# Optimization experiments

Hardware: AMD Instinct MI355X
Metric: run time of the kernel (lower is better)

## Reference

```python
import jax, jax.numpy as jnp
from jax import lax
import numpy as np

DN = ('NCHW', 'OIHW', 'NCHW')

def _conv(x, w, b, s, p):
    out = lax.conv_general_dilated(x, w, (s, s), ((p, p), (p, p)), dimension_numbers=DN)
    return out + b[None, :, None, None]

def _convt(x, w, b):
    # torch ConvTranspose2d(k=3, stride=2, pad=1, out_pad=1) == lhs-dilated conv
    # with flipped kernel, pad (k-1-p, k-1-p+op) = (1, 2). Doubles H, W.
    wk = jnp.flip(w, (2, 3)).transpose(1, 0, 2, 3)  # [Cin,Cout,k,k] -> [Cout,Cin,k,k]
    out = lax.conv_general_dilated(x, wk, (1, 1), ((1, 2), (1, 2)), lhs_dilation=(2, 2), dimension_numbers=DN)
    return out + b[None, :, None, None]

def _bn(x, g, b):
    # training-mode batch stats over (N, H, W), eps=1e-5
    m = jnp.mean(x, (0, 2, 3), keepdims=True)
    v = jnp.var(x, (0, 2, 3), keepdims=True)
    return (x - m) * lax.rsqrt(v + 1e-5) * g[None, :, None, None] + b[None, :, None, None]

def _hsw(x):
    return x * jnp.clip(x + 3.0, 0.0, 6.0) * (1.0 / 6.0)

SCORE_THRESHOLD = 0.6
DOWN_SCALE = 4.0

def _forward(feature, ch_w1, ch_b1, ch_w2, ch_b2, ch_w3, ch_b3, ch_g1, ch_be1, ch_g2, ch_be2,
             cl_w1, cl_b1, cl_w2, cl_b2, cl_g, cl_be, cl_dw, cl_db,
             rg_tw, rg_tb, rg_g, rg_be, rg_w, rg_b, hm_tw, hm_tb):
    # ---- CommonHead (note: original reuses bn1 after both stride-2 convs) ----
    h = _bn(_conv(feature, ch_w1, ch_b1, 2, 1), ch_g1, ch_be1)   # [B,192,64,64]
    h = _bn(_conv(h, ch_w2, ch_b2, 2, 1), ch_g1, ch_be1)         # [B,192,32,32]
    h = _hsw(_bn(_conv(h, ch_w3, ch_b3, 1, 0), ch_g2, ch_be2))   # [B,32,32,32]
    # ---- PageClassifyNet ----
    c = _hsw(_bn(_conv(h, cl_w1, cl_b1, 1, 1), cl_g, cl_be))     # [B,32,32,32]
    c = _conv(c, cl_w2, cl_b2, 1, 1)                             # [B,1,32,32]
    cls = c.reshape(c.shape[0], -1) @ cl_dw.T + cl_db            # [B,2]
    r = _hsw(_bn(_convt(feature, rg_tw, rg_tb), rg_g, rg_be))    # [B,32,256,256]
    reg = _conv(r, rg_w, rg_b, 1, 1)                             # [B,2,256,256]
    # ---- AuxiliaryHeatmapNet ----
    hm = _convt(feature, hm_tw, hm_tb)                           # [B,8,256,256]
    # ---- keypoint decode (threshold + argmax + gather), vectorized over batch ----
    B, _, H, W = hm.shape
    flat = hm.transpose(0, 2, 3, 1).reshape(B, H * W, 8)          # HWC layout as in source
    pages = jnp.stack([flat[..., :4], flat[..., 4:]], axis=1)     # [B,2(pages),HW,4(corners)]
    idx = jnp.argmax(pages, axis=2)                               # [B,2,4] flat spatial index
    y_idx = (idx // W).astype(reg.dtype)
    x_idx = (idx % W).astype(reg.dtype)
    fi = idx.reshape(B, -1)                                       # [B,8]
    reg_flat = reg.reshape(B, 2, H * W)
    off_x = jnp.take_along_axis(reg_flat[:, 0, :], fi, axis=1).reshape(B, 2, 4)
    off_y = jnp.take_along_axis(reg_flat[:, 1, :], fi, axis=1).reshape(B, 2, 4)
    xs = jnp.clip((off_x + x_idx) * DOWN_SCALE / (W * DOWN_SCALE), 0.0, 1.0)
    ys = jnp.clip((off_y + y_idx) * DOWN_SCALE / (H * DOWN_SCALE), 0.0, 1.0)
    valid = cls > SCORE_THRESHOLD                                 # [B,2]
    label = jnp.broadcast_to(jnp.arange(2, dtype=xs.dtype)[None, :], (B, 2))
    row = jnp.concatenate([label[..., None], xs, ys], axis=-1)    # [B,2,9]
    return jnp.where(valid[..., None], row, jnp.asarray(-1.0, xs.dtype))


def setup_inputs() -> dict:
    key = jax.random.key(0)
    ks = jax.random.split(key, 32)
    rn = lambda k, shp, s=0.05: jax.random.normal(k, shp, dtype=jnp.float32) * s
    d = {}
    d['feature'] = jax.random.normal(ks[0], (8, 512, 128, 128), dtype=jnp.float32)
    d['ch_w1'] = rn(ks[1], (192, 512, 3, 3)); d['ch_b1'] = rn(ks[2], (192,))
    d['ch_w2'] = rn(ks[3], (192, 192, 3, 3)); d['ch_b2'] = rn(ks[4], (192,))
    d['ch_w3'] = rn(ks[5], (32, 192, 1, 1)); d['ch_b3'] = rn(ks[6], (32,))
    d['ch_g1'] = jnp.ones((192,), jnp.float32); d['ch_be1'] = jnp.zeros((192,), jnp.float32)
    d['ch_g2'] = jnp.ones((32,), jnp.float32); d['ch_be2'] = jnp.zeros((32,), jnp.float32)
    d['cl_w1'] = rn(ks[7], (32, 32, 3, 3)); d['cl_b1'] = rn(ks[8], (32,))
    d['cl_w2'] = rn(ks[9], (1, 32, 3, 3)); d['cl_b2'] = rn(ks[10], (1,))
    d['cl_g'] = jnp.ones((32,), jnp.float32); d['cl_be'] = jnp.zeros((32,), jnp.float32)
    d['cl_dw'] = rn(ks[11], (2, 1024), 0.1); d['cl_db'] = rn(ks[12], (2,))
    d['rg_tw'] = rn(ks[13], (512, 32, 3, 3)); d['rg_tb'] = rn(ks[14], (32,))
    d['rg_g'] = jnp.ones((32,), jnp.float32); d['rg_be'] = jnp.zeros((32,), jnp.float32)
    d['rg_w'] = rn(ks[15], (2, 32, 3, 3)); d['rg_b'] = rn(ks[16], (2,))
    d['hm_tw'] = rn(ks[17], (512, 8, 3, 3)); d['hm_tb'] = rn(ks[18], (8,))
    return d


def reference(feature, ch_w1, ch_b1, ch_w2, ch_b2, ch_w3, ch_b3, ch_g1, ch_be1, ch_g2, ch_be2,
              cl_w1, cl_b1, cl_w2, cl_b2, cl_g, cl_be, cl_dw, cl_db,
              rg_tw, rg_tb, rg_g, rg_be, rg_w, rg_b, hm_tw, hm_tb):
    return _forward(feature, ch_w1, ch_b1, ch_w2, ch_b2, ch_w3, ch_b3, ch_g1, ch_be1, ch_g2, ch_be2,
                    cl_w1, cl_b1, cl_w2, cl_b2, cl_g, cl_be, cl_dw, cl_db,
                    rg_tw, rg_tb, rg_g, rg_be, rg_w, rg_b, hm_tw, hm_tb)
```

## Files before the change

kernel.cpp:

```cpp
#include <hip/hip_runtime.h>

typedef unsigned short u16;
typedef u16 u16x4 __attribute__((ext_vector_type(4)));
typedef u16 u16x8 __attribute__((ext_vector_type(8)));
typedef __bf16 bf16x8 __attribute__((ext_vector_type(8)));
typedef float f32x4 __attribute__((ext_vector_type(4)));

__device__ __forceinline__ float bf2f(u16 v) {
  unsigned u = ((unsigned)v) << 16;
  return __builtin_bit_cast(float, u);
}
__device__ __forceinline__ u16 f2bf(float f) {
  unsigned u = __builtin_bit_cast(unsigned, f);
  u += 0x7FFFu + ((u >> 16) & 1u);
  return (u16)(u >> 16);
}
__device__ __forceinline__ float hsw(float v) {
  return v * fminf(fmaxf(v + 3.f, 0.f), 6.f) * (1.f / 6.f);
}
__device__ __forceinline__ f32x4 mfma16(u16x8 a, u16x8 b, f32x4 c) {
  return __builtin_amdgcn_mfma_f32_16x16x32_bf16(
      __builtin_bit_cast(bf16x8, a), __builtin_bit_cast(bf16x8, b), c, 0, 0, 0);
}

#define LR 40

__global__ __launch_bounds__(256) void k_tobf(const float* __restrict__ f,
                                              u16* __restrict__ fbh) {
  __shared__ float tl[64 * 65];
  const int t = threadIdx.x;
  const int bid = blockIdx.x;
  const int ict = bid & 7, xt = (bid >> 3) & 1, y = (bid >> 4) & 127, n = bid >> 11;
  const int x0 = xt * 64, ic0 = ict * 64;
#pragma unroll
  for (int i = 0; i < 4; ++i) {
    const int e = t + i * 256;
    const int icl = e >> 4, xq = e & 15;
    const f32x4 v =
        *(const f32x4*)&f[((n * 512 + ic0 + icl) * 128 + y) * 128 + x0 + xq * 4];
#pragma unroll
    for (int j = 0; j < 4; ++j) tl[icl * 65 + xq * 4 + j] = v[j];
  }
  __syncthreads();
#pragma unroll
  for (int i = 0; i < 4; ++i) {
    const int e = t + i * 256;
    const int xl = e >> 4;
    const int icg = (e & 15) * 4;
    u16x4 v;
#pragma unroll
    for (int j = 0; j < 4; ++j) v[j] = f2bf(tl[(icg + j) * 65 + xl]);
    *(u16x4*)&fbh[(((size_t)((n * 128 + y) * 128 + x0 + xl)) << 9) + ic0 + icg] = v;
  }
}

__global__ __launch_bounds__(256) void k_pack_all(const float* __restrict__ w1,
                                                  const float* __restrict__ w2,
                                                  const float* __restrict__ rgw,
                                                  const float* __restrict__ hmw,
                                                  u16* __restrict__ bp1,
                                                  u16* __restrict__ bp2,
                                                  u16* __restrict__ bp5) {
  const int b = blockIdx.x;
  if (b < 3456) {
    const int e = b * 256 + threadIdx.x;
    const int ici = e & 31;
    const int rest = e >> 5;
    const int oc = rest % 192;
    const int kc = rest / 192;
    const int icc = kc & 15, tap = kc >> 4;
    const int ic = icc * 32 + ici;
    bp1[e] = f2bf(w1[(oc * 512 + ic) * 9 + tap]);
  } else if (b < 4752) {
    const int e = (b - 3456) * 256 + threadIdx.x;
    const int ici = e & 31;
    const int rest = e >> 5;
    const int oc = rest % 192;
    const int kc = rest / 192;
    const int icc = kc % 6, tap = kc / 6;
    const int ic = icc * 32 + ici;
    bp2[e] = f2bf(w2[(oc * 192 + ic) * 9 + tap]);
  } else {
    const int e = (b - 4752) * 256 + threadIdx.x;
    const int ici = e & 31;
    const int rest = e >> 5;
    const int oc = rest % 48;
    const int sic = rest / 48;
    const int icc = sic & 15, slot = sic >> 4;
    const int ic = icc * 32 + ici;
    const int kytab[9] = {1, 1, 1, 2, 0, 2, 2, 0, 0};
    const int kxtab[9] = {1, 2, 0, 1, 1, 2, 0, 2, 0};
    const int ky = kytab[slot], kx = kxtab[slot];
    float v = 0.f;
    if (oc < 32)
      v = rgw[((ic * 32 + oc) * 3 + ky) * 3 + kx];
    else if (oc < 40)
      v = hmw[((ic * 8 + (oc - 32)) * 3 + ky) * 3 + kx];
    bp5[e] = f2bf(v);
  }
}

__global__ __launch_bounds__(256) void k_conv1(const u16* __restrict__ fbh,
                                               const u16* __restrict__ bph,
                                               const float* __restrict__ bias,
                                               u16* __restrict__ y1) {
  __shared__ u16 Al[64 * LR];
  __shared__ u16 Bl[192 * LR];
  __shared__ float bl[192];
  const int t = threadIdx.x;
  const int n = blockIdx.x >> 6, oy = blockIdx.x & 63;
  if (t < 192) bl[t] = bias[t];
  const int lane = t & 63, wv = t >> 6;
  const int row = lane & 15, g = lane >> 4;
  const int oxs = t >> 2, icq = t & 3;
  const f32x4 z4 = {0.f, 0.f, 0.f, 0.f};
  f32x4 acc[4][3];
#pragma unroll
  for (int i = 0; i < 4; ++i)
#pragma unroll
    for (int j = 0; j < 3; ++j) acc[i][j] = z4;

#define C1_LOAD(KC, AV, BV)                                                    \
  {                                                                            \
    const int tap_ = (KC) >> 4, icc_ = (KC)&15;                                \
    const int ky_ = tap_ / 3, kx_ = tap_ - ky_ * 3;                            \
    const int iy_ = 2 * oy - 1 + ky_;                                          \
    const int ix_ = 2 * oxs - 1 + kx_;                                         \
    u16x8 v_ = {0, 0, 0, 0, 0, 0, 0, 0};                                       \
    if ((unsigned)iy_ < 128u && (unsigned)ix_ < 128u)                          \
      v_ = *(const u16x8*)&fbh[((size_t)((n * 128 + iy_) * 128 + ix_) << 9) +  \
                               icc_ * 32 + icq * 8];                           \
    AV = v_;                                                                   \
    const size_t bbase_ = (size_t)(tap_ * 16 + icc_) * (192 * 32);             \
    _Pragma("unroll") for (int i_ = 0; i_ < 3; ++i_) {                         \
      const int e_ = t + i_ * 256;                                             \
      BV[i_] = *(const u16x8*)&bph[bbase_ + (e_ >> 2) * 32 + (e_ & 3) * 8];    \
    }                                                                          \
  }

  u16x8 avA, bvA[3], avB, bvB[3];
  C1_LOAD(0, avA, bvA);

  for (int kc = 0; kc < 144; ++kc) {
    __syncthreads();
    *(u16x8*)&Al[oxs * LR + icq * 8] = avA;
#pragma unroll
    for (int i = 0; i < 3; ++i) {
      const int e = t + i * 256;
      *(u16x8*)&Bl[(e >> 2) * LR + (e & 3) * 8] = bvA[i];
    }
    __syncthreads();
    if (kc < 143) C1_LOAD(kc + 1, avB, bvB);
    u16x8 af[4], bf[3];
#pragma unroll
    for (int mf = 0; mf < 4; ++mf)
      af[mf] = *(const u16x8*)&Al[(mf * 16 + row) * LR + g * 8];
#pragma unroll
    for (int nf = 0; nf < 3; ++nf)
      bf[nf] = *(const u16x8*)&Bl[(wv * 48 + nf * 16 + row) * LR + g * 8];
#pragma unroll
    for (int mf = 0; mf < 4; ++mf)
#pragma unroll
      for (int nf = 0; nf < 3; ++nf) acc[mf][nf] = mfma16(af[mf], bf[nf], acc[mf][nf]);
    avA = avB;
#pragma unroll
    for (int i = 0; i < 3; ++i) bvA[i] = bvB[i];
  }
#undef C1_LOAD
#pragma unroll
  for (int mf = 0; mf < 4; ++mf)
#pragma unroll
    for (int nf = 0; nf < 3; ++nf)
#pragma unroll
      for (int r = 0; r < 4; ++r) {
        const int m = mf * 16 + g * 4 + r;
        const int oc = wv * 48 + nf * 16 + row;
        y1[((n * 64 + oy) * 64 + m) * 192 + oc] = f2bf(acc[mf][nf][r] + bl[oc]);
      }
}

__global__ __launch_bounds__(256) void k_conv2(const u16* __restrict__ y1,
                                               const u16* __restrict__ bph,
                                               const float* __restrict__ bias,
                                               const float* __restrict__ sc,
                                               const float* __restrict__ sh,
                                               float* __restrict__ y2) {
  __shared__ u16 Al[64 * LR];
  __shared__ u16 Bl[192 * LR];
  __shared__ float bl[192], scl[192], shl[192];
  const int t = threadIdx.x;
  const int n = blockIdx.x >> 4, oyp = blockIdx.x & 15;
  if (t < 192) {
    bl[t] = bias[t];
    scl[t] = sc[t];
    shl[t] = sh[t];
  }
  __syncthreads();
  const int lane = t & 63, wv = t >> 6;
  const int row = lane & 15, g = lane >> 4;
  const int ms = t >> 2, icq = t & 3;
  const int ryr = ms >> 5, oxs = ms & 31;
  const f32x4 z4 = {0.f, 0.f, 0.f, 0.f};
  f32x4 acc[4][3];
#pragma unroll
  for (int i = 0; i < 4; ++i)
#pragma unroll
    for (int j = 0; j < 3; ++j) acc[i][j] = z4;

#define C2_LOAD(KC, RAW, OK, BV)                                               \
  {                                                                            \
    const int tap_ = (KC) / 6, icc_ = (KC)-tap_ * 6;                           \
    const int ky_ = tap_ / 3, kx_ = tap_ - ky_ * 3;                            \
    const int iy_ = 2 * (oyp * 2 + ryr) - 1 + ky_;                             \
    const int ix_ = 2 * oxs - 1 + kx_;                                         \
    OK = ((unsigned)iy_ < 64u) && ((unsigned)ix_ < 64u);                       \
    u16x8 v_ = {0, 0, 0, 0, 0, 0, 0, 0};                                       \
    if (OK)                                                                    \
      v_ = *(const u16x8*)&y1[((n * 64 + iy_) * 64 + ix_) * 192 + icc_ * 32 +  \
                              icq * 8];                                        \
    RAW = v_;                                                                  \
    const size_t bbase_ = (size_t)(tap_ * 6 + icc_) * (192 * 32);              \
    _Pragma("unroll") for (int i_ = 0; i_ < 3; ++i_) {                         \
      const int e_ = t + i_ * 256;                                             \
      BV[i_] = *(const u16x8*)&bph[bbase_ + (e_ >> 2) * 32 + (e_ & 3) * 8];    \
    }                                                                          \
  }

  u16x8 rawA, bvA[3], rawB, bvB[3];
  bool okA, okB;
  C2_LOAD(0, rawA, okA, bvA);

  for (int kc = 0; kc < 54; ++kc) {
    const int tap = kc / 6, icc = kc - tap * 6;
    const int icb = icc * 32 + icq * 8;
    u16x8 av = {0, 0, 0, 0, 0, 0, 0, 0};
    if (okA) {
#pragma unroll
      for (int j = 0; j < 8; ++j)
        av[j] = f2bf(bf2f(rawA[j]) * scl[icb + j] + shl[icb + j]);
    }
    __syncthreads();
    *(u16x8*)&Al[ms * LR + icq * 8] = av;
#pragma unroll
    for (int i = 0; i < 3; ++i) {
      const int e = t + i * 256;
      *(u16x8*)&Bl[(e >> 2) * LR + (e & 3) * 8] = bvA[i];
    }
    __syncthreads();
    if (kc < 53) C2_LOAD(kc + 1, rawB, okB, bvB);
    u16x8 af[4], bf[3];
#pragma unroll
    for (int mf = 0; mf < 4; ++mf)
      af[mf] = *(const u16x8*)&Al[(mf * 16 + row) * LR + g * 8];
#pragma unroll
    for (int nf = 0; nf < 3; ++nf)
      bf[nf] = *(const u16x8*)&Bl[(wv * 48 + nf * 16 + row) * LR + g * 8];
#pragma unroll
    for (int mf = 0; mf < 4; ++mf)
#pragma unroll
      for (int nf = 0; nf < 3; ++nf) acc[mf][nf] = mfma16(af[mf], bf[nf], acc[mf][nf]);
    rawA = rawB;
    okA = okB;
#pragma unroll
    for (int i = 0; i < 3; ++i) bvA[i] = bvB[i];
  }
#undef C2_LOAD
#pragma unroll
  for (int mf = 0; mf < 4; ++mf)
#pragma unroll
    for (int nf = 0; nf < 3; ++nf)
#pragma unroll
      for (int r = 0; r < 4; ++r) {
        const int m = mf * 16 + g * 4 + r;
        const int oy = oyp * 2 + (m >> 5), ox = m & 31;
        const int oc = wv * 48 + nf * 16 + row;
        y2[((n * 32 + oy) * 32 + ox) * 192 + oc] = acc[mf][nf][r] + bl[oc];
      }
}

#define AST 40
#define ARS (130 * 40)
#define BST 40
__global__ __launch_bounds__(256) void k_convt(const u16* __restrict__ fbh,
                                               const u16* __restrict__ bph,
                                               const float* __restrict__ rgb,
                                               const float* __restrict__ hmb,
                                               u16* __restrict__ rr,
                                               float* __restrict__ hm) {
  __shared__ u16 AH[2 * ARS];
  __shared__ u16 BH[9 * 48 * BST];
  const int t = threadIdx.x;
  const int bid = (blockIdx.x & 7) * 128 + (blockIdx.x >> 3);
  const int n = bid >> 7, iyb = bid & 127;
  const int lane = t & 63, wv = t >> 6;
  const int row = lane & 15, g = lane >> 4;

  if (t < 8) {
    const int r = t >> 2, j = t & 3;
    const u16x8 z = {0, 0, 0, 0, 0, 0, 0, 0};
    *(u16x8*)&AH[r * ARS + 128 * AST + j * 8] = z;
  }

  float bias3[3];
#pragma unroll
  for (int nf = 0; nf < 3; ++nf) {
    const int oc = nf * 16 + row;
    bias3[nf] = (oc < 32) ? rgb[oc] : ((oc < 40) ? hmb[oc - 32] : 0.f);
  }

  const int SCt[9] = {0, 1, 1, 2, 2, 3, 3, 3, 3};
  const int SDt[9] = {0, 0, 0, 0, 1, 0, 0, 1, 1};
  const int SXt[9] = {0, 0, 1, 0, 0, 0, 1, 0, 1};

  int rr_[4], px_[4], iq_[4];
#pragma unroll
  for (int i = 0; i < 4; ++i) {
    const int u = t + i * 256;
    rr_[i] = u >> 9;
    px_[i] = (u >> 2) & 127;
    iq_[i] = u & 3;
  }

  const f32x4 z4 = {0.f, 0.f, 0.f, 0.f};
  f32x4 acc[4][2][3];
#pragma unroll
  for (int c = 0; c < 4; ++c)
#pragma unroll
    for (int m = 0; m < 2; ++m)
#pragma unroll
      for (int j = 0; j < 3; ++j) acc[c][m][j] = z4;

#define LOAD_A(ICC, DST)                                                       \
  _Pragma("unroll") for (int i = 0; i < 4; ++i) {                              \
    const int iy = iyb + rr_[i];                                               \
    u16x8 v = {0, 0, 0, 0, 0, 0, 0, 0};                                        \
    if (iy < 128)                                                              \
      v = *(const u16x8*)&fbh[((size_t)((n * 128 + iy) * 128 + px_[i]) << 9) + \
                              (ICC)*32 + iq_[i] * 8];                          \
    DST[i] = v;                                                                \
  }

#define LOAD_B(ICC, DST)                                                       \
  _Pragma("unroll") for (int i = 0; i < 7; ++i) {                              \
    const int e = t + i * 256;                                                 \
    u16x8 v = {0, 0, 0, 0, 0, 0, 0, 0};                                        \
    if (e < 1728) {                                                            \
      const int slot = e / 192, rem = e % 192;                                 \
      const int oc = rem >> 2, icq = rem & 3;                                  \
      v = *(const u16x8*)&bph[((size_t)((slot * 16 + (ICC)) * 48 + oc) << 5) + \
                              icq * 8];                                        \
    }                                                                          \
    DST[i] = v;                                                                \
  }

  u16x8 ahA[4], bhA[7], ahB[4], bhB[7];
  LOAD_A(0, ahA);
  LOAD_B(0, bhA);

  for (int icc = 0; icc < 16; ++icc) {
    __syncthreads();
#pragma unroll
    for (int i = 0; i < 4; ++i)
      *(u16x8*)&AH[rr_[i] * ARS + px_[i] * AST + iq_[i] * 8] = ahA[i];
#pragma unroll
    for (int i = 0; i < 7; ++i) {
      const int e = t + i * 256;
      if (e < 1728) {
        const int slot = e / 192, rem = e % 192;
        const int oc = rem >> 2, icq = rem & 3;
        *(u16x8*)&BH[(slot * 48 + oc) * BST + icq * 8] = bhA[i];
      }
    }
    __syncthreads();

    if (icc < 15) {
      LOAD_A(icc + 1, ahB);
      LOAD_B(icc + 1, bhB);
    }

#pragma unroll
    for (int slot = 0; slot < 9; ++slot) {
      const int cls = SCt[slot], diy = SDt[slot], dix = SXt[slot];
      const u16x8 bf0 = *(const u16x8*)&BH[(slot * 48 + row) * BST + g * 8];
      const u16x8 bf1 = *(const u16x8*)&BH[(slot * 48 + 16 + row) * BST + g * 8];
      const u16x8 bf2 = *(const u16x8*)&BH[(slot * 48 + 32 + row) * BST + g * 8];
#pragma unroll
      for (int mfl = 0; mfl < 2; ++mfl) {
        const int mf = wv * 2 + mfl;
        const u16x8 af =
            *(const u16x8*)&AH[diy * ARS + (mf * 16 + row + dix) * AST + g * 8];
        acc[cls][mfl][0] = mfma16(af, bf0, acc[cls][mfl][0]);
        acc[cls][mfl][1] = mfma16(af, bf1, acc[cls][mfl][1]);
        acc[cls][mfl][2] = mfma16(af, bf2, acc[cls][mfl][2]);
      }
    }

#pragma unroll
    for (int i = 0; i < 4; ++i) ahA[i] = ahB[i];
#pragma unroll
    for (int i = 0; i < 7; ++i) bhA[i] = bhB[i];
  }
#undef LOAD_A
#undef LOAD_B

#pragma unroll
  for (int cls = 0; cls < 4; ++cls) {
    const int oy = 2 * iyb + (cls >> 1);
    const int xp = cls & 1;
#pragma unroll
    for (int mfl = 0; mfl < 2; ++mfl)
#pragma unroll
      for (int nf = 0; nf < 3; ++nf)
#pragma unroll
        for (int r = 0; r < 4; ++r) {
          const int m = (wv * 2 + mfl) * 16 + g * 4 + r;
          const int ox = 2 * m + xp;
          const int oc = nf * 16 + row;
          const float v = acc[cls][mfl][nf][r] + bias3[nf];
          if (oc < 32)
            rr[((size_t)((n * 256 + oy) * 256 + ox)) * 32 + oc] = f2bf(v);
          else if (oc < 40)
            hm[(size_t)(n * 8 + (oc - 32)) * 65536 + oy * 256 + ox] = v;
        }
  }
}

template <int CG, bool BF16>
__global__ __launch_bounds__(256) void k_statsf(
    const void* __restrict__ in_, int M, int PB, float* __restrict__ gsum,
    float* __restrict__ gsq, int* __restrict__ counter,
    const float* __restrict__ g, const float* __restrict__ be, float invM,
    float* __restrict__ sc, float* __restrict__ sh) {
  const int C = CG * 32;
  __shared__ float red[8][CG * 32];
  __shared__ int lastBlk;
  const int t = threadIdx.x;
  const int pg = t >> 5, ln = t & 31;
  float s[CG], q[CG];
#pragma unroll
  for (int c = 0; c < CG; ++c) { s[c] = 0.f; q[c] = 0.f; }
  const int p0 = blockIdx.x * PB;
  const int pend = min(p0 + PB, M);
  for (int p = p0 + pg; p < pend; p += 8) {
#pragma unroll
    for (int c = 0; c < CG; ++c) {
      float v;
      if (BF16)
        v = bf2f(((const u16*)in_)[(size_t)p * C + c * 32 + ln]);
      else
        v = ((const float*)in_)[(size_t)p * C + c * 32 + ln];
      s[c] += v;
      q[c] += v * v;
    }
  }
#pragma unroll
  for (int c = 0; c < CG; ++c) red[pg][c * 32 + ln] = s[c];
  __syncthreads();
  if (t < C) {
    float tot = 0.f;
#pragma unroll
    for (int k = 0; k < 8; ++k) tot += red[k][t];
    atomicAdd(&gsum[t], tot);
  }
  __syncthreads();
#pragma unroll
  for (int c = 0; c < CG; ++c) red[pg][c * 32 + ln] = q[c];
  __syncthreads();
  if (t < C) {
    float tot = 0.f;
#pragma unroll
    for (int k = 0; k < 8; ++k) tot += red[k][t];
    atomicAdd(&gsq[t], tot);
  }
  __syncthreads();
  if (t == 0) {
    __threadfence();
    lastBlk = (atomicAdd(counter, 1) == (int)gridDim.x - 1) ? 1 : 0;
  }
  __syncthreads();
  if (lastBlk) {
    __threadfence();
    if (t < C) {
      const float m = gsum[t] * invM;
      const float var = gsq[t] * invM - m * m;
      const float inv = rsqrtf(var + 1e-5f);
      const float sg = g[t] * inv;
      sc[t] = sg;
      sh[t] = be[t] - m * sg;
    }
  }
}

__global__ __launch_bounds__(256) void k_conv3(const float* __restrict__ y2,
                                               const float* __restrict__ w3,
                                               const float* __restrict__ b3,
                                               const float* __restrict__ sc,
                                               const float* __restrict__ sh,
                                               float* __restrict__ y3) {
  __shared__ float wl[32 * 192];
  __shared__ float scl[192], shl[192];
  const int t = threadIdx.x;
  for (int e = t; e < 6144; e += 256) wl[e] = w3[e];
  if (t < 192) {
    scl[t] = sc[t];
    shl[t] = sh[t];
  }
  __syncthreads();
  const int px = blockIdx.x * 256 + t;
  float acc[32];
#pragma unroll
  for (int oc = 0; oc < 32; ++oc) acc[oc] = 0.f;
  const float* base = &y2[(size_t)px * 192];
  for (int icb = 0; icb < 192; icb += 8) {
    const f32x4 r0 = *(const f32x4*)&base[icb];
    const f32x4 r1 = *(const f32x4*)&base[icb + 4];
    float v[8];
#pragma unroll
    for (int j = 0; j < 8; ++j) {
      const float r = (j < 4) ? r0[j & 3] : r1[j & 3];
      v[j] = r * scl[icb + j] + shl[icb + j];
    }
#pragma unroll
    for (int oc = 0; oc < 32; ++oc) {
      const f32x4 w0 = *(const f32x4*)&wl[oc * 192 + icb];
      const f32x4 w1 = *(const f32x4*)&wl[oc * 192 + icb + 4];
      acc[oc] += v[0] * w0[0] + v[1] * w0[1] + v[2] * w0[2] + v[3] * w0[3] +
                 v[4] * w1[0] + v[5] * w1[1] + v[6] * w1[2] + v[7] * w1[3];
    }
  }
#pragma unroll
  for (int oc = 0; oc < 32; ++oc) y3[(size_t)px * 32 + oc] = acc[oc] + b3[oc];
}

__global__ __launch_bounds__(256) void k_clsconv1(const float* __restrict__ y3,
                                                  const float* __restrict__ w1,
                                                  const float* __restrict__ b1,
                                                  const float* __restrict__ sc,
                                                  const float* __restrict__ sh,
                                                  float* __restrict__ c1) {
  __shared__ float wl[9216];
  __shared__ float scl[32], shl[32];
  const int t = threadIdx.x;
  for (int e = t; e < 9216; e += 256) {
    const int oc = e & 31;
    const int tmp = e >> 5;
    const int tap = tmp % 9, ic = tmp / 9;
    wl[e] = w1[(oc * 32 + ic) * 9 + tap];
  }
  if (t < 32) {
    scl[t] = sc[t];
    shl[t] = sh[t];
  }
  __syncthreads();
  const int px = blockIdx.x * 64 + (t & 63);
  const int ocg = t >> 6;
  const int n = px >> 10, y0 = (px >> 5) & 31, x0 = px & 31;
  float acc[8];
#pragma unroll
  for (int j = 0; j < 8; ++j) acc[j] = 0.f;
  for (int tap = 0; tap < 9; ++tap) {
    const int dy = tap / 3 - 1, dx = tap % 3 - 1;
    const int yy = y0 + dy, xx = x0 + dx;
    if ((unsigned)yy < 32u && (unsigned)xx < 32u) {
      const float* ib = &y3[((n << 10) + yy * 32 + xx) * 32];
      for (int ic = 0; ic < 32; ++ic) {
        const float v = hsw(ib[ic] * scl[ic] + shl[ic]);
        const float* wp = &wl[(ic * 9 + tap) * 32 + ocg * 8];
#pragma unroll
        for (int j = 0; j < 8; ++j) acc[j] += v * wp[j];
      }
    }
  }
#pragma unroll
  for (int j = 0; j < 8; ++j) c1[px * 32 + ocg * 8 + j] = acc[j] + b1[ocg * 8 + j];
}

__global__ __launch_bounds__(256) void k_cls(const float* __restrict__ c1,
                                             const float* __restrict__ w2,
                                             const float* __restrict__ b2,
                                             const float* __restrict__ dw,
                                             const float* __restrict__ db,
                                             const float* __restrict__ sc,
                                             const float* __restrict__ sh,
                                             float* __restrict__ cls) {
  __shared__ float wl[288];
  __shared__ float scl[32], shl[32];
  __shared__ float red0[256], red1[256];
  const int t = threadIdx.x;
  const int n = blockIdx.x;
  for (int e = t; e < 288; e += 256) wl[e] = w2[e];
  if (t < 32) {
    scl[t] = sc[t];
    shl[t] = sh[t];
  }
  __syncthreads();
  float s0 = 0.f, s1 = 0.f;
  for (int i = 0; i < 4; ++i) {
    const int px = i * 256 + t;
    const int y0 = px >> 5, x0 = px & 31;
    float c2 = b2[0];
    for (int tap = 0; tap < 9; ++tap) {
      const int dy = tap / 3 - 1, dx = tap % 3 - 1;
      const int yy = y0 + dy, xx = x0 + dx;
      if ((unsigned)yy < 32u && (unsigned)xx < 32u) {
        const float* ib = &c1[((n << 10) + yy * 32 + xx) * 32];
        for (int ic = 0; ic < 32; ++ic)
          c2 += hsw(ib[ic] * scl[ic] + shl[ic]) * wl[ic * 9 + tap];
      }
    }
    s0 += c2 * dw[px];
    s1 += c2 * dw[1024 + px];
  }
  red0[t] = s0;
  red1[t] = s1;
  __syncthreads();
  for (int s = 128; s; s >>= 1) {
    if (t < s) {
      red0[t] += red0[t + s];
      red1[t] += red1[t + s];
    }
    __syncthreads();
  }
  if (t == 0) {
    cls[n * 2 + 0] = red0[0] + db[0];
    cls[n * 2 + 1] = red1[0] + db[1];
  }
}

__global__ __launch_bounds__(256) void k_regconv(const u16* __restrict__ rr,
                                                 const float* __restrict__ w,
                                                 const float* __restrict__ b,
                                                 const float* __restrict__ sc,
                                                 const float* __restrict__ sh,
                                                 float* __restrict__ reg) {
  __shared__ u16 rl[3 * 258 * 33];
  __shared__ float wl[576];
  __shared__ float scl[32], shl[32];
  const int t = threadIdx.x;
  const int n = blockIdx.x >> 8, oy = blockIdx.x & 255;
  for (int e = t; e < 576; e += 256) wl[e] = w[e];
  if (t < 32) {
    scl[t] = sc[t];
    shl[t] = sh[t];
  }
  if (t < 192) {
    const int ry = t / 64, side = (t >> 5) & 1, ic = t & 31;
    rl[(ry * 258 + side * 257) * 33 + ic] = 0;
  }
  __syncthreads();
  for (int e = t; e < 3072; e += 256) {
    const int icq8 = e & 3;
    const int pxx = (e >> 2) & 255;
    const int ry = e >> 10;
    const int rowi = oy - 1 + ry;
    u16x8 raw = {0, 0, 0, 0, 0, 0, 0, 0};
    bool ok = (unsigned)rowi < 256u;
    if (ok)
      raw = *(const u16x8*)&rr[((size_t)((n * 256 + rowi) * 256 + pxx)) * 32 + icq8 * 8];
#pragma unroll
    for (int j = 0; j < 8; ++j) {
      const int ic = icq8 * 8 + j;
      float v = 0.f;
      if (ok) v = hsw(bf2f(raw[j]) * scl[ic] + shl[ic]);
      rl[(ry * 258 + pxx + 1) * 33 + ic] = f2bf(v);
    }
  }
  __syncthreads();
  const int px = t;
  float a0 = b[0], a1 = b[1];
#pragma unroll
  for (int ry = 0; ry < 3; ++ry)
#pragma unroll
    for (int kx = 0; kx < 3; ++kx) {
      const u16* ib = &rl[(ry * 258 + px + kx) * 33];
      for (int ic = 0; ic < 32; ++ic) {
        const float v = bf2f(ib[ic]);
        a0 += v * wl[ic * 9 + ry * 3 + kx];
        a1 += v * wl[288 + ic * 9 + ry * 3 + kx];
      }
    }
  reg[(n * 2 + 0) * 65536 + oy * 256 + px] = a0;
  reg[(n * 2 + 1) * 65536 + oy * 256 + px] = a1;
}

__global__ __launch_bounds__(256) void k_argmaxfin(const float* __restrict__ hm,
                                                   int* __restrict__ idx,
                                                   int* __restrict__ counter,
                                                   const float* __restrict__ cls,
                                                   const float* __restrict__ reg,
                                                   float* __restrict__ out) {
  __shared__ float bv[256];
  __shared__ int bi[256];
  __shared__ int lastBlk;
  const int t = threadIdx.x;
  const float* base = &hm[(size_t)blockIdx.x * 65536];
  float best = -3.402823466e38f;
  int bidx = 2147483647;
  for (int i = t; i < 65536; i += 256) {
    const float v = base[i];
    if (v > best) {
      best = v;
      bidx = i;
    }
  }
  bv[t] = best;
  bi[t] = bidx;
  __syncthreads();
  for (int s = 128; s; s >>= 1) {
    if (t < s) {
      if (bv[t + s] > bv[t] || (bv[t + s] == bv[t] && bi[t + s] < bi[t])) {
        bv[t] = bv[t + s];
        bi[t] = bi[t + s];
      }
    }
    __syncthreads();
  }
  if (t == 0) {
    idx[blockIdx.x] = bi[0];
    __threadfence();
    lastBlk = (atomicAdd(counter, 1) == (int)gridDim.x - 1) ? 1 : 0;
  }
  __syncthreads();
  if (lastBlk) {
    __threadfence();
    if (t < 16) {
      const int n = t >> 1, p = t & 1;
      const float cv = cls[n * 2 + p];
      float* o = &out[(n * 2 + p) * 9];
      if (!(cv > 0.6f)) {
        for (int i = 0; i < 9; ++i) o[i] = -1.f;
      } else {
        o[0] = (float)p;
        for (int c = 0; c < 4; ++c) {
          const int id = idx[n * 8 + p * 4 + c];
          const int yi = id >> 8, xi = id & 255;
          const float ox_ = reg[(n * 2 + 0) * 65536 + id];
          const float oy_ = reg[(n * 2 + 1) * 65536 + id];
          o[1 + c] = fminf(fmaxf((ox_ + (float)xi) * (1.f / 256.f), 0.f), 1.f);
          o[5 + c] = fminf(fmaxf((oy_ + (float)yi) * (1.f / 256.f), 0.f), 1.f);
        }
      }
    }
  }
}

extern "C" void kernel_launch(void* const* d_in, const int* in_sizes, int n_in,
                              void* d_out, int out_size, void* d_ws, size_t ws_size,
                              hipStream_t stream) {
  const float* feature = (const float*)d_in[0];
  const float* ch_w1 = (const float*)d_in[1];
  const float* ch_b1 = (const float*)d_in[2];
  const float* ch_w2 = (const float*)d_in[3];
  const float* ch_b2 = (const float*)d_in[4];
  const float* ch_w3 = (const float*)d_in[5];
  const float* ch_b3 = (const float*)d_in[6];
  const float* ch_g1 = (const float*)d_in[7];
  const float* ch_be1 = (const float*)d_in[8];
  const float* ch_g2 = (const float*)d_in[9];
  const float* ch_be2 = (const float*)d_in[10];
  const float* cl_w1 = (const float*)d_in[11];
  const float* cl_b1 = (const float*)d_in[12];
  const float* cl_w2 = (const float*)d_in[13];
  const float* cl_b2 = (const float*)d_in[14];
  const float* cl_g = (const float*)d_in[15];
  const float* cl_be = (const float*)d_in[16];
  const float* cl_dw = (const float*)d_in[17];
  const float* cl_db = (const float*)d_in[18];
  const float* rg_tw = (const float*)d_in[19];
  const float* rg_tb = (const float*)d_in[20];
  const float* rg_g = (const float*)d_in[21];
  const float* rg_be = (const float*)d_in[22];
  const float* rg_w = (const float*)d_in[23];
  const float* rg_b = (const float*)d_in[24];
  const float* hm_tw = (const float*)d_in[25];
  const float* hm_tb = (const float*)d_in[26];
  float* out = (float*)d_out;

  char* w = (char*)d_ws;
  const size_t OFF_FB = 0;
  const size_t OFF_BP1 = 134217728;
  const size_t OFF_BP2 = 135987200;
  const size_t OFF_BP5 = 136650752;
  const size_t OFF_Y1 = 137093120;
  const size_t OFF_Y2 = 149676032;
  const size_t OFF_Y3 = 155967488;
  const size_t OFF_C1 = 157016064;
  const size_t OFF_RR = 158064640;
  const size_t OFF_HM = 191619072;
  const size_t OFF_REG = 208396288;
  const size_t OFF_STATS = 212590592;
  const size_t OFF_PARAMS = 212594496;
  const size_t OFF_CLS = 212598336;
  const size_t OFF_IDX = 212598400;
  const size_t WS_NEED = 212598656;
  if (ws_size < WS_NEED) return;

  u16* FB = (u16*)(w + OFF_FB);
  u16* BP1 = (u16*)(w + OFF_BP1);
  u16* BP2 = (u16*)(w + OFF_BP2);
  u16* BP5 = (u16*)(w + OFF_BP5);
  u16* Y1 = (u16*)(w + OFF_Y1);
  float* Y2 = (float*)(w + OFF_Y2);
  float* Y3 = (float*)(w + OFF_Y3);
  float* C1 = (float*)(w + OFF_C1);
  u16* RR = (u16*)(w + OFF_RR);
  float* HM = (float*)(w + OFF_HM);
  float* REG = (float*)(w + OFF_REG);
  float* GSUM = (float*)(w + OFF_STATS);
  float* GSQ = GSUM + 480;
  int* CNT = (int*)(w + OFF_STATS + 3840);
  float* SC = (float*)(w + OFF_PARAMS);
  float* SH = SC + 480;
  float* CLS = (float*)(w + OFF_CLS);
  int* IDX = (int*)(w + OFF_IDX);

  (void)hipMemsetAsync(w + OFF_STATS, 0, 3904, stream);

  k_tobf<<<16384, 256, 0, stream>>>(feature, FB);
  k_pack_all<<<5616, 256, 0, stream>>>(ch_w1, ch_w2, rg_tw, hm_tw, BP1, BP2, BP5);

  k_conv1<<<512, 256, 0, stream>>>(FB, BP1, ch_b1, Y1);
  k_statsf<6, true><<<128, 256, 0, stream>>>(Y1, 32768, 256, GSUM + 0, GSQ + 0,
                                             CNT + 0, ch_g1, ch_be1, 1.f / 32768.f,
                                             SC + 0, SH + 0);
  k_conv2<<<128, 256, 0, stream>>>(Y1, BP2, ch_b2, SC + 0, SH + 0, Y2);
  k_statsf<6, false><<<32, 256, 0, stream>>>(Y2, 8192, 256, GSUM + 192, GSQ + 192,
                                             CNT + 1, ch_g1, ch_be1, 1.f / 8192.f,
                                             SC + 192, SH + 192);
  k_conv3<<<32, 256, 0, stream>>>(Y2, ch_w3, ch_b3, SC + 192, SH + 192, Y3);
  k_statsf<1, false><<<8, 256, 0, stream>>>(Y3, 8192, 1024, GSUM + 384, GSQ + 384,
                                            CNT + 2, ch_g2, ch_be2, 1.f / 8192.f,
                                            SC + 384, SH + 384);
  k_clsconv1<<<128, 256, 0, stream>>>(Y3, cl_w1, cl_b1, SC + 384, SH + 384, C1);
  k_statsf<1, false><<<8, 256, 0, stream>>>(C1, 8192, 1024, GSUM + 416, GSQ + 416,
                                            CNT + 3, cl_g, cl_be, 1.f / 8192.f,
                                            SC + 416, SH + 416);
  k_cls<<<8, 256, 0, stream>>>(C1, cl_w2, cl_b2, cl_dw, cl_db, SC + 416, SH + 416,
                               CLS);
  k_convt<<<1024, 256, 0, stream>>>(FB, BP5, rg_tb, hm_tb, RR, HM);
  k_statsf<1, true><<<256, 256, 0, stream>>>(RR, 524288, 2048, GSUM + 448, GSQ + 448,
                                             CNT + 4, rg_g, rg_be, 1.f / 524288.f,
                                             SC + 448, SH + 448);
  k_regconv<<<2048, 256, 0, stream>>>(RR, rg_w, rg_b, SC + 448, SH + 448, REG);
  k_argmaxfin<<<64, 256, 0, stream>>>(HM, IDX, CNT + 5, CLS, REG, out);
}
```

Measured before the change: 809.5 us.

## Fuse BatchNorm statistics into conv1, conv2 and convT epilogues

Each of the three conv kernels now accumulates per-channel sum and sum-of-squares in its epilogue. Partials are reduced in shared memory, then added atomically to global buffers, and the last block computes the BN scale and shift. This removes three separate stats kernels, their launches, and the re-read of the conv outputs (the convT output is large). In exchange it adds global atomics, fence and counter logic to each conv, and computes the stats from fp32 values instead of the rounded bf16 stored outputs.

Measured after the change: 768.5 us. 5.1% less time.

```diff
diff --git a/kernel.cpp b/kernel.cpp
--- a/kernel.cpp
+++ b/kernel.cpp
@@ -103,13 +103,26 @@
 __global__ __launch_bounds__(256) void k_conv1(const u16* __restrict__ fbh,
                                                const u16* __restrict__ bph,
                                                const float* __restrict__ bias,
-                                               u16* __restrict__ y1) {
+                                               u16* __restrict__ y1,
+                                               float* __restrict__ gsum,
+                                               float* __restrict__ gsq,
+                                               int* __restrict__ counter,
+                                               const float* __restrict__ g1,
+                                               const float* __restrict__ be1,
+                                               float* __restrict__ sc,
+                                               float* __restrict__ sh) {
   __shared__ u16 Al[64 * LR];
   __shared__ u16 Bl[192 * LR];
   __shared__ float bl[192];
+  __shared__ float ssum[192], ssq[192];
+  __shared__ int lastBlk;
   const int t = threadIdx.x;
   const int n = blockIdx.x >> 6, oy = blockIdx.x & 63;
-  if (t < 192) bl[t] = bias[t];
+  if (t < 192) {
+    bl[t] = bias[t];
+    ssum[t] = 0.f;
+    ssq[t] = 0.f;
+  }
   const int lane = t & 63, wv = t >> 6;
   const int row = lane & 15, g = lane >> 4;
   const int oxs = t >> 2, icq = t & 3;
@@ -167,6 +180,8 @@
     for (int i = 0; i < 3; ++i) bvA[i] = bvB[i];
   }
 #undef C1_LOAD
+
+  float s3[3] = {0.f, 0.f, 0.f}, q3[3] = {0.f, 0.f, 0.f};
 #pragma unroll
   for (int mf = 0; mf < 4; ++mf)
 #pragma unroll
@@ -175,25 +190,67 @@
       for (int r = 0; r < 4; ++r) {
         const int m = mf * 16 + g * 4 + r;
         const int oc = wv * 48 + nf * 16 + row;
-        y1[((n * 64 + oy) * 64 + m) * 192 + oc] = f2bf(acc[mf][nf][r] + bl[oc]);
+        const float v = acc[mf][nf][r] + bl[oc];
+        y1[((n * 64 + oy) * 64 + m) * 192 + oc] = f2bf(v);
+        s3[nf] += v;
+        q3[nf] += v * v;
       }
+#pragma unroll
+  for (int nf = 0; nf < 3; ++nf) {
+    const int oc = wv * 48 + nf * 16 + row;
+    atomicAdd(&ssum[oc], s3[nf]);
+    atomicAdd(&ssq[oc], q3[nf]);
+  }
+  __syncthreads();
+  if (t < 192) {
+    atomicAdd(&gsum[t], ssum[t]);
+    atomicAdd(&gsq[t], ssq[t]);
+  }
+  __syncthreads();
+  if (t == 0) {
+    __threadfence();
+    lastBlk = (atomicAdd(counter, 1) == (int)gridDim.x - 1) ? 1 : 0;
+  }
+  __syncthreads();
+  if (lastBlk) {
+    __threadfence();
+    if (t < 192) {
+      const float m = gsum[t] * (1.f / 32768.f);
+      const float var = gsq[t] * (1.f / 32768.f) - m * m;
+      const float inv = rsqrtf(var + 1e-5f);
+      const float sg = g1[t] * inv;
+      sc[t] = sg;
+      sh[t] = be1[t] - m * sg;
+    }
+  }
 }
 
 __global__ __launch_bounds__(256) void k_conv2(const u16* __restrict__ y1,
                                                const u16* __restrict__ bph,
                                                const float* __restrict__ bias,
-                                               const float* __restrict__ sc,
-                                               const float* __restrict__ sh,
-                                               float* __restrict__ y2) {
+                                               const float* __restrict__ sc_in,
+                                               const float* __restrict__ sh_in,
+                                               float* __restrict__ y2,
+                                               float* __restrict__ gsum,
+                                               float* __restrict__ gsq,
+                                               int* __restrict__ counter,
+                                               const float* __restrict__ g1,
+                                               const float* __restrict__ be1,
+                                               float* __restrict__ sc,
+                                               float* __restrict__ sh) {
   __shared__ u16 Al[64 * LR];
   __shared__ u16 Bl[192 * LR];
   __shared__ float bl[192], scl[192], shl[192];
+  __shared__ float ssum[192], ssq[192];
+  __shared__ int lastBlk;
   const int t = threadIdx.x;
   const int n = blockIdx.x >> 4, oyp = blockIdx.x & 15;
   if (t < 192) {
     bl[t] = bias[t];
-    scl[t] = sc[t];
-    shl[t] = sh[t];
+    scl[t] = sc_in[t];
+    shl[t] = sh_in[t];
+    ssum[t] = 0.f;
+    ssq[t] = 0.f;
   }
   __syncthreads();
   const int lane = t & 63, wv = t >> 6;
@@ -265,6 +322,8 @@
     for (int i = 0; i < 3; ++i) bvA[i] = bvB[i];
   }
 #undef C2_LOAD
+
+  float s3[3] = {0.f, 0.f, 0.f}, q3[3] = {0.f, 0.f, 0.f};
 #pragma unroll
   for (int mf = 0; mf < 4; ++mf)
 #pragma unroll
@@ -274,8 +333,39 @@
         const int m = mf * 16 + g * 4 + r;
         const int oy = oyp * 2 + (m >> 5), ox = m & 31;
         const int oc = wv * 48 + nf * 16 + row;
-        y2[((n * 32 + oy) * 32 + ox) * 192 + oc] = acc[mf][nf][r] + bl[oc];
+        const float v = acc[mf][nf][r] + bl[oc];
+        y2[((n * 32 + oy) * 32 + ox) * 192 + oc] = v;
+        s3[nf] += v;
+        q3[nf] += v * v;
       }
+#pragma unroll
+  for (int nf = 0; nf < 3; ++nf) {
+    const int oc = wv * 48 + nf * 16 + row;
+    atomicAdd(&ssum[oc], s3[nf]);
+    atomicAdd(&ssq[oc], q3[nf]);
+  }
+  __syncthreads();
+  if (t < 192) {
+    atomicAdd(&gsum[t], ssum[t]);
+    atomicAdd(&gsq[t], ssq[t]);
+  }
+  __syncthreads();
+  if (t == 0) {
+    __threadfence();
+    lastBlk = (atomicAdd(counter, 1) == (int)gridDim.x - 1) ? 1 : 0;
+  }
+  __syncthreads();
+  if (lastBlk) {
+    __threadfence();
+    if (t < 192) {
+      const float m = gsum[t] * (1.f / 8192.f);
+      const float var = gsq[t] * (1.f / 8192.f) - m * m;
+      const float inv = rsqrtf(var + 1e-5f);
+      const float sg = g1[t] * inv;
+      sc[t] = sg;
+      sh[t] = be1[t] - m * sg;
+    }
+  }
 }
 
 #define AST 40
@@ -286,9 +376,18 @@
                                                const float* __restrict__ rgb,
                                                const float* __restrict__ hmb,
                                                u16* __restrict__ rr,
-                                               float* __restrict__ hm) {
+                                               float* __restrict__ hm,
+                                               float* __restrict__ gsum,
+                                               float* __restrict__ gsq,
+                                               int* __restrict__ counter,
+                                               const float* __restrict__ rg_g,
+                                               const float* __restrict__ rg_be,
+                                               float* __restrict__ sc,
+                                               float* __restrict__ sh) {
   __shared__ u16 AH[2 * ARS];
   __shared__ u16 BH[9 * 48 * BST];
+  __shared__ float ssum[32], ssq[32];
+  __shared__ int lastBlk;
   const int t = threadIdx.x;
   const int bid = (blockIdx.x & 7) * 128 + (blockIdx.x >> 3);
   const int n = bid >> 7, iyb = bid & 127;
@@ -299,6 +398,10 @@
     const int r = t >> 2, j = t & 3;
     const u16x8 z = {0, 0, 0, 0, 0, 0, 0, 0};
     *(u16x8*)&AH[r * ARS + 128 * AST + j * 8] = z;
+  }
+  if (t < 32) {
+    ssum[t] = 0.f;
+    ssq[t] = 0.f;
   }
 
   float bias3[3];
@@ -403,6 +506,7 @@
 #undef LOAD_A
 #undef LOAD_B
 
+  float s2[2] = {0.f, 0.f}, q2[2] = {0.f, 0.f};
 #pragma unroll
   for (int cls = 0; cls < 4; ++cls) {
     const int oy = 2 * iyb + (cls >> 1);
@@ -417,11 +521,40 @@
           const int ox = 2 * m + xp;
           const int oc = nf * 16 + row;
           const float v = acc[cls][mfl][nf][r] + bias3[nf];
-          if (oc < 32)
+          if (oc < 32) {
             rr[((size_t)((n * 256 + oy) * 256 + ox)) * 32 + oc] = f2bf(v);
-          else if (oc < 40)
+            s2[nf] += v;
+            q2[nf] += v * v;
+          } else if (oc < 40)
             hm[(size_t)(n * 8 + (oc - 32)) * 65536 + oy * 256 + ox] = v;
         }
+  }
+#pragma unroll
+  for (int nf = 0; nf < 2; ++nf) {
+    atomicAdd(&ssum[nf * 16 + row], s2[nf]);
+    atomicAdd(&ssq[nf * 16 + row], q2[nf]);
+  }
+  __syncthreads();
+  if (t < 32) {
+    atomicAdd(&gsum[t], ssum[t]);
+    atomicAdd(&gsq[t], ssq[t]);
+  }
+  __syncthreads();
+  if (t == 0) {
+    __threadfence();
+    lastBlk = (atomicAdd(counter, 1) == (int)gridDim.x - 1) ? 1 : 0;
+  }
+  __syncthreads();
+  if (lastBlk) {
+    __threadfence();
+    if (t < 32) {
+      const float m = gsum[t] * (1.f / 524288.f);
+      const float var = gsq[t] * (1.f / 524288.f) - m * m;
+      const float inv = rsqrtf(var + 1e-5f);
+      const float sg = rg_g[t] * inv;
+      sc[t] = sg;
+      sh[t] = rg_be[t] - m * sg;
+    }
   }
 }
 
@@ -819,14 +952,11 @@
   k_tobf<<<16384, 256, 0, stream>>>(feature, FB);
   k_pack_all<<<5616, 256, 0, stream>>>(ch_w1, ch_w2, rg_tw, hm_tw, BP1, BP2, BP5);
 
-  k_conv1<<<512, 256, 0, stream>>>(FB, BP1, ch_b1, Y1);
-  k_statsf<6, true><<<128, 256, 0, stream>>>(Y1, 32768, 256, GSUM + 0, GSQ + 0,
-                                             CNT + 0, ch_g1, ch_be1, 1.f / 32768.f,
-                                             SC + 0, SH + 0);
-  k_conv2<<<128, 256, 0, stream>>>(Y1, BP2, ch_b2, SC + 0, SH + 0, Y2);
-  k_statsf<6, false><<<32, 256, 0, stream>>>(Y2, 8192, 256, GSUM + 192, GSQ + 192,
-                                             CNT + 1, ch_g1, ch_be1, 1.f / 8192.f,
-                                             SC + 192, SH + 192);
+  k_conv1<<<512, 256, 0, stream>>>(FB, BP1, ch_b1, Y1, GSUM + 0, GSQ + 0, CNT + 0,
+                                   ch_g1, ch_be1, SC + 0, SH + 0);
+  k_conv2<<<128, 256, 0, stream>>>(Y1, BP2, ch_b2, SC + 0, SH + 0, Y2, GSUM + 192,
+                                   GSQ + 192, CNT + 1, ch_g1, ch_be1, SC + 192,
+                                   SH + 192);
   k_conv3<<<32, 256, 0, stream>>>(Y2, ch_w3, ch_b3, SC + 192, SH + 192, Y3);
   k_statsf<1, false><<<8, 256, 0, stream>>>(Y3, 8192, 1024, GSUM + 384, GSQ + 384,
                                             CNT + 2, ch_g2, ch_be2, 1.f / 8192.f,
@@ -837,10 +967,9 @@
                                             SC + 416, SH + 416);
   k_cls<<<8, 256, 0, stream>>>(C1, cl_w2, cl_b2, cl_dw, cl_db, SC + 416, SH + 416,
                                CLS);
-  k_convt<<<1024, 256, 0, stream>>>(FB, BP5, rg_tb, hm_tb, RR, HM);
-  k_statsf<1, true><<<256, 256, 0, stream>>>(RR, 524288, 2048, GSUM + 448, GSQ + 448,
-                                             CNT + 4, rg_g, rg_be, 1.f / 524288.f,
-                                             SC + 448, SH + 448);
+  k_convt<<<1024, 256, 0, stream>>>(FB, BP5, rg_tb, hm_tb, RR, HM, GSUM + 448,
+                                    GSQ + 448, CNT + 4, rg_g, rg_be, SC + 448,
+                                    SH + 448);
   k_regconv<<<2048, 256, 0, stream>>>(RR, rg_w, rg_b, SC + 448, SH + 448, REG);
   k_argmaxfin<<<64, 256, 0, stream>>>(HM, IDX, CNT + 5, CLS, REG, out);
 }
```
